# Kernel tuning notes

Measured on AMD Instinct MI355X. Metric: run time of the kernel, lower is better.

Reference implementation:

```python
import jax, jax.numpy as jnp
import numpy as np

N, E, D_IN, D_OUT, R, B = 50000, 800000, 64, 64, 10, 4

def setup_inputs() -> dict:
    key = jax.random.key(0)
    ks = jax.random.split(key, 8)
    feat = jax.random.normal(ks[0], (N, D_IN), jnp.float32)
    src = jax.random.randint(ks[1], (E,), 0, N)
    dst = jax.random.randint(ks[2], (E,), 0, N)
    etype = jax.random.randint(ks[3], (E,), 0, R)
    norm = jax.random.uniform(ks[4], (E,), jnp.float32)
    weight = jax.random.normal(ks[5], (B, D_IN, D_OUT), jnp.float32) * 0.1
    w_comp = jax.random.normal(ks[6], (R, B), jnp.float32) * 0.1
    self_loop_weight = jax.random.normal(ks[7], (D_IN, D_OUT), jnp.float32) * 0.1
    return dict(feat=feat, src=src, dst=dst, etype=etype, norm=norm,
                weight=weight, w_comp=w_comp, self_loop_weight=self_loop_weight)

def reference(feat, src, dst, etype, norm, weight, w_comp, self_loop_weight):
    # Basis decomposition: per-relation weight W_r = sum_b w_comp[r,b] * weight[b]
    W = jnp.einsum('rb,bio->rio', w_comp, weight)            # [R, D_in, D_out]
    # Transform all nodes under every relation (R is small), then gather per edge.
    # This avoids materializing an [E, D_in, D_out] per-edge weight tensor.
    xr = jnp.einsum('ni,rio->rno', feat, W)                  # [R, N, D_out]
    msg = xr[etype, src] * norm[:, None]                     # [E, D_out]
    # Scatter-aggregate messages into destination nodes (DGL sum aggregator).
    agg = jax.ops.segment_sum(msg, dst, num_segments=N)      # [N, D_out]
    # SumAggregator adds curr_emb = dst_feat @ self_loop_weight to the msg sum.
    h = feat @ self_loop_weight + agg                        # [N, D_out]
    return jax.nn.relu(h)
```

## Files before the change

kernel.cpp:

```cpp
#include <hip/hip_runtime.h>
#include <hip/hip_bf16.h>
#include <stdint.h>

#define NN 50000
#define EE 800000
#define DD 64
#define RR 10
#define BB 4
#define NPAD 50176
#define NBKT 391
#define TBLK 4301
#define BBLK 196
#define SORT_CAP 7168
#define FCAP 4096

using u16 = unsigned short;
using u32 = unsigned int;

typedef short v8s __attribute__((ext_vector_type(8)));
typedef float v4f __attribute__((ext_vector_type(4)));

__device__ __forceinline__ u32 f2bf_rn(float x) {
    u32 u = __float_as_uint(x);
    return (u + 0x7FFFu + ((u >> 16) & 1u)) >> 16;
}
__device__ __forceinline__ u32 pack2bf(float a, float b) {
    return f2bf_rn(a) | (f2bf_rn(b) << 16);
}

__global__ __launch_bounds__(256, 2)
void k_big(const float* __restrict__ feat,
           const float* __restrict__ weight,
           const float* __restrict__ w_comp,
           const float* __restrict__ self_w,
           const int* __restrict__ src, const int* __restrict__ dst,
           const int* __restrict__ etype, const float* __restrict__ norm,
           int* __restrict__ bcur, int* __restrict__ flag,
           uint2* __restrict__ rec,
           u16* __restrict__ xr, float* __restrict__ out,
           int tcount, int tb_off, int cap) {
    __shared__ __align__(16) char smem[34816];
    const int t = threadIdx.x;

    if ((int)blockIdx.x >= tcount) {
        int* lh  = (int*)smem;
        int* gb  = lh + 392;
        int* lcc = gb + 392;
        const int ebase = ((int)blockIdx.x - tcount) * 4096;
        for (int b = t; b < 392; b += 256) { lh[b] = 0; lcc[b] = 0; }
        __syncthreads();
        #pragma unroll 4
        for (int j = 0; j < 16; ++j) {
            int e = ebase + t + 256 * j;
            if (e < EE) atomicAdd(&lh[dst[e] >> 7], 1);
        }
        __syncthreads();
        for (int b = t; b < 392; b += 256) {
            int c = lh[b];
            gb[b] = c ? atomicAdd(&bcur[b], c) : 0;
        }
        __syncthreads();
        #pragma unroll 4
        for (int j = 0; j < 16; ++j) {
            int e = ebase + t + 256 * j;
            if (e < EE) {
                int d = dst[e];
                int b = d >> 7;
                int p = atomicAdd(&lcc[b], 1);
                int idx = gb[b] + p;
                u32 w0 = (u32)src[e] | ((u32)etype[e] << 16) | ((u32)(d & 127) << 20);
                if (cap == 0 || idx < (b + 1) * cap)
                    rec[idx] = make_uint2(w0, __float_as_uint(norm[e]));
                else
                    atomicOr(&flag[b], 2);
            }
        }
        return;
    }

    u16*   sWt = (u16*)smem;
    u16*   sFb = (u16*)(smem + 9216);
    float* sD  = (float*)smem;

    const int tb = (int)blockIdx.x + tb_off;
    const int r = tb / 391;
    const int nbase = (tb % 391) * 128;

    if (r < RR) {
        const float c0 = w_comp[r * BB + 0];
        const float c1 = w_comp[r * BB + 1];
        const float c2 = w_comp[r * BB + 2];
        const float c3 = w_comp[r * BB + 3];
        #pragma unroll
        for (int qq = 0; qq < 16; ++qq) {
            int idx = t + 256 * qq;
            int n = idx & 63, k = idx >> 6;
            float v = c0 * weight[k * 64 + n] + c1 * weight[4096 + k * 64 + n] +
                      c2 * weight[8192 + k * 64 + n] + c3 * weight[12288 + k * 64 + n];
            sWt[n * 72 + k] = (u16)f2bf_rn(v);
        }
    } else {
        #pragma unroll
        for (int qq = 0; qq < 16; ++qq) {
            int idx = t + 256 * qq;
            int n = idx & 63, k = idx >> 6;
            sWt[n * 72 + k] = (u16)f2bf_rn(self_w[k * 64 + n]);
        }
    }

    #pragma unroll
    for (int qq = 0; qq < 8; ++qq) {
        int f4 = qq * 256 + t;
        int nl = f4 >> 4;
        int ic = (f4 & 15) << 2;
        int n = nbase + nl;
        float4 v = make_float4(0.f, 0.f, 0.f, 0.f);
        if (n < NN) v = reinterpret_cast<const float4*>(feat)[(size_t)n * 16 + (f4 & 15)];
        *reinterpret_cast<uint2*>(&sFb[nl * 72 + ic]) =
            make_uint2(pack2bf(v.x, v.y), pack2bf(v.z, v.w));
    }
    __syncthreads();

    const int wv = t >> 6;
    const int L = t & 63;
    const int q = L >> 4;
    const int c = L & 15;

    v8s bf[4][2];
    #pragma unroll
    for (int nt = 0; nt < 4; ++nt)
        #pragma unroll
        for (int kh = 0; kh < 2; ++kh)
            bf[nt][kh] = *reinterpret_cast<const v8s*>(&sWt[(nt * 16 + c) * 72 + kh * 32 + q * 8]);

    v8s af[2][2];
    #pragma unroll
    for (int mt = 0; mt < 2; ++mt) {
        int row = wv * 32 + mt * 16 + c;
        #pragma unroll
        for (int kh = 0; kh < 2; ++kh)
            af[mt][kh] = *reinterpret_cast<const v8s*>(&sFb[row * 72 + kh * 32 + q * 8]);
    }
    __syncthreads();

    v4f acc[2][4];
    #pragma unroll
    for (int mt = 0; mt < 2; ++mt)
        #pragma unroll
        for (int nt = 0; nt < 4; ++nt) {
            acc[mt][nt] = (v4f)(0.f);
            #pragma unroll
            for (int kh = 0; kh < 2; ++kh)
                acc[mt][nt] = __builtin_amdgcn_mfma_f32_16x16x32_bf16(
                    af[mt][kh], bf[nt][kh], acc[mt][nt], 0, 0, 0);
        }

    #pragma unroll
    for (int mt = 0; mt < 2; ++mt) {
        int mrow = wv * 32 + mt * 16 + q * 4;
        #pragma unroll
        for (int nt = 0; nt < 4; ++nt)
            #pragma unroll
            for (int rg = 0; rg < 4; ++rg)
                sD[(mrow + rg) * 68 + nt * 16 + c] = acc[mt][nt][rg];
    }
    __syncthreads();

    const int row = t >> 1;
    const int cb = (t & 1) * 32;
    const int g = nbase + row;
    if (g < NN) {
        const float* sp = &sD[row * 68 + cb];
        if (r < RR) {
            u16* dp = xr + ((size_t)r * NN + g) * DD + cb;
            #pragma unroll
            for (int j = 0; j < 4; ++j) {
                float4 f0 = *reinterpret_cast<const float4*>(sp + j * 8);
                float4 f1 = *reinterpret_cast<const float4*>(sp + j * 8 + 4);
                uint4 o;
                o.x = pack2bf(f0.x, f0.y);
                o.y = pack2bf(f0.z, f0.w);
                o.z = pack2bf(f1.x, f1.y);
                o.w = pack2bf(f1.z, f1.w);
                *reinterpret_cast<uint4*>(dp + j * 8) = o;
            }
        } else {
            float* dp = out + (size_t)g * DD + cb;
            #pragma unroll
            for (int j = 0; j < 8; ++j)
                *reinterpret_cast<float4*>(dp + j * 4) =
                    *reinterpret_cast<const float4*>(sp + j * 4);
        }
    }
}

__global__ __launch_bounds__(256)
void k_init(int* __restrict__ bcur, int* __restrict__ flag) {
    int t = blockIdx.x * 256 + threadIdx.x;
    if (t < 392) { bcur[t] = t * FCAP; flag[t] = 0; }
}

__global__ __launch_bounds__(256)
void k_bhist(const int* __restrict__ dst, int* __restrict__ bktcnt) {
    __shared__ int lh[NBKT];
    const int t = threadIdx.x;
    for (int b = t; b < NBKT; b += 256) lh[b] = 0;
    __syncthreads();
    const int ebase = blockIdx.x * 8192;
    #pragma unroll
    for (int j = 0; j < 32; ++j) {
        int e = ebase + t + 256 * j;
        if (e < EE) atomicAdd(&lh[dst[e] >> 7], 1);
    }
    __syncthreads();
    for (int b = t; b < NBKT; b += 256) {
        int v = lh[b];
        if (v) atomicAdd(&bktcnt[b], v);
    }
}

__global__ __launch_bounds__(512)
void k_bscan(const int* __restrict__ bktcnt, int* __restrict__ bktbase,
             int* __restrict__ bcur, int* __restrict__ flag) {
    __shared__ int s[512];
    int t = threadIdx.x;
    int v = (t < NBKT) ? bktcnt[t] : 0;
    s[t] = v;
    __syncthreads();
    #pragma unroll
    for (int off = 1; off < 512; off <<= 1) {
        int x = (t >= off) ? s[t - off] : 0;
        __syncthreads();
        s[t] += x;
        __syncthreads();
    }
    if (t < 392) {
        int b = s[t] - v;
        bktbase[t] = b;
        bcur[t] = b;
        flag[t] = 0;
    }
}

__global__ __launch_bounds__(512)
void k_sortb2(const int* __restrict__ bcurF, const int* __restrict__ bktbase,
              int* __restrict__ flag, uint2* __restrict__ rec,
              int* __restrict__ base, int* __restrict__ cnt, int cap) {
    __shared__ uint2 buf[SORT_CAP];
    __shared__ int h[128];
    __shared__ int sc[128];
    __shared__ int lc[128];
    const int b = blockIdx.x;
    const int t = threadIdx.x;
    const int seg0 = cap ? b * cap : bktbase[b];
    const int cnt_b = bcurF[b] - seg0;
    if (flag[b] & 2) return;
    if (cnt_b > SORT_CAP) {
        if (t == 0) flag[b] = 1;
        return;
    }
    if (t < 128) h[t] = 0;
    __syncthreads();
    for (int k = t; k < cnt_b; k += 512) {
        uint2 rr = rec[seg0 + k];
        buf[k] = rr;
        atomicAdd(&h[(rr.x >> 20) & 127], 1);
    }
    __syncthreads();
    if (t < 128) sc[t] = h[t];
    __syncthreads();
    #pragma unroll
    for (int off = 1; off < 128; off <<= 1) {
        int x = 0;
        if (t < 128 && t >= off) x = sc[t - off];
        __syncthreads();
        if (t < 128) sc[t] += x;
        __syncthreads();
    }
    if (t < 128) {
        int ex = sc[t] - h[t];
        lc[t] = ex;
        base[b * 128 + t] = seg0 + ex;
        cnt[b * 128 + t] = h[t];
    }
    __syncthreads();
    for (int k = t; k < cnt_b; k += 512) {
        uint2 rr = buf[k];
        int p = atomicAdd(&lc[(rr.x >> 20) & 127], 1);
        rec[seg0 + p] = rr;
    }
}

__global__ __launch_bounds__(256)
void k_agg(const int* __restrict__ base, const int* __restrict__ cnt,
           const uint2* __restrict__ rec, const u16* __restrict__ xr,
           const int* __restrict__ flag, const int* __restrict__ bktbase,
           const int* __restrict__ bcurF,
           const int* __restrict__ src, const int* __restrict__ dst,
           const int* __restrict__ etype, const float* __restrict__ norm,
           int cap, float* __restrict__ out) {
    int n = (blockIdx.x * 256 + threadIdx.x) >> 6;
    int L = threadIdx.x & 63;
    if (n >= NN) return;
    const int g = L >> 4;
    const int c = L & 15;
    float a0 = 0.f, a1 = 0.f, a2 = 0.f, a3 = 0.f;
    const int fb = flag[n >> 7];

    if (__builtin_expect(fb == 0, 1)) {
        int st = base[n];
        int cn = cnt[n];
        int k = 0;
        for (; k + 16 <= cn; k += 16) {
            uint2 r0 = rec[st + k + g];
            uint2 r1 = rec[st + k + 4 + g];
            uint2 r2 = rec[st + k + 8 + g];
            uint2 r3 = rec[st + k + 12 + g];
            size_t w0 = ((size_t)((r0.x >> 16) & 0xFu) * NN + (r0.x & 0xFFFFu)) * DD;
            size_t w1 = ((size_t)((r1.x >> 16) & 0xFu) * NN + (r1.x & 0xFFFFu)) * DD;
            size_t w2 = ((size_t)((r2.x >> 16) & 0xFu) * NN + (r2.x & 0xFFFFu)) * DD;
            size_t w3 = ((size_t)((r3.x >> 16) & 0xFu) * NN + (r3.x & 0xFFFFu)) * DD;
            uint2 u0 = *reinterpret_cast<const uint2*>(&xr[w0 + 4 * c]);
            uint2 u1 = *reinterpret_cast<const uint2*>(&xr[w1 + 4 * c]);
            uint2 u2 = *reinterpret_cast<const uint2*>(&xr[w2 + 4 * c]);
            uint2 u3 = *reinterpret_cast<const uint2*>(&xr[w3 + 4 * c]);
            float n0 = __uint_as_float(r0.y), n1 = __uint_as_float(r1.y);
            float n2 = __uint_as_float(r2.y), n3 = __uint_as_float(r3.y);
            a0 = fmaf(__uint_as_float((u0.x & 0xFFFFu) << 16), n0, a0);
            a1 = fmaf(__uint_as_float(u0.x & 0xFFFF0000u), n0, a1);
            a2 = fmaf(__uint_as_float((u0.y & 0xFFFFu) << 16), n0, a2);
            a3 = fmaf(__uint_as_float(u0.y & 0xFFFF0000u), n0, a3);
            a0 = fmaf(__uint_as_float((u1.x & 0xFFFFu) << 16), n1, a0);
            a1 = fmaf(__uint_as_float(u1.x & 0xFFFF0000u), n1, a1);
            a2 = fmaf(__uint_as_float((u1.y & 0xFFFFu) << 16), n1, a2);
            a3 = fmaf(__uint_as_float(u1.y & 0xFFFF0000u), n1, a3);
            a0 = fmaf(__uint_as_float((u2.x & 0xFFFFu) << 16), n2, a0);
            a1 = fmaf(__uint_as_float(u2.x & 0xFFFF0000u), n2, a1);
            a2 = fmaf(__uint_as_float((u2.y & 0xFFFFu) << 16), n2, a2);
            a3 = fmaf(__uint_as_float(u2.y & 0xFFFF0000u), n2, a3);
            a0 = fmaf(__uint_as_float((u3.x & 0xFFFFu) << 16), n3, a0);
            a1 = fmaf(__uint_as_float(u3.x & 0xFFFF0000u), n3, a1);
            a2 = fmaf(__uint_as_float((u3.y & 0xFFFFu) << 16), n3, a2);
            a3 = fmaf(__uint_as_float(u3.y & 0xFFFF0000u), n3, a3);
        }
        for (int kk = k + g; kk < cn; kk += 4) {
            uint2 rr = rec[st + kk];
            size_t rw = ((size_t)((rr.x >> 16) & 0xFu) * NN + (rr.x & 0xFFFFu)) * DD;
            uint2 u = *reinterpret_cast<const uint2*>(&xr[rw + 4 * c]);
            float nm = __uint_as_float(rr.y);
            a0 = fmaf(__uint_as_float((u.x & 0xFFFFu) << 16), nm, a0);
            a1 = fmaf(__uint_as_float(u.x & 0xFFFF0000u), nm, a1);
            a2 = fmaf(__uint_as_float((u.y & 0xFFFFu) << 16), nm, a2);
            a3 = fmaf(__uint_as_float(u.y & 0xFFFF0000u), nm, a3);
        }
    } else if (fb & 2) {
        for (int e = g; e < EE; e += 4) {
            if (dst[e] == n) {
                size_t rw = ((size_t)etype[e] * NN + src[e]) * DD;
                uint2 u = *reinterpret_cast<const uint2*>(&xr[rw + 4 * c]);
                float nm = norm[e];
                a0 = fmaf(__uint_as_float((u.x & 0xFFFFu) << 16), nm, a0);
                a1 = fmaf(__uint_as_float(u.x & 0xFFFF0000u), nm, a1);
                a2 = fmaf(__uint_as_float((u.y & 0xFFFFu) << 16), nm, a2);
                a3 = fmaf(__uint_as_float(u.y & 0xFFFF0000u), nm, a3);
            }
        }
    } else {
        int b = n >> 7;
        int seg0 = cap ? b * cap : bktbase[b];
        int segend = bcurF[b];
        int my = n & 127;
        for (int k = seg0 + g; k < segend; k += 4) {
            uint2 rr = rec[k];
            if (((rr.x >> 20) & 127) == (u32)my) {
                size_t rw = ((size_t)((rr.x >> 16) & 0xFu) * NN + (rr.x & 0xFFFFu)) * DD;
                uint2 u = *reinterpret_cast<const uint2*>(&xr[rw + 4 * c]);
                float nm = __uint_as_float(rr.y);
                a0 = fmaf(__uint_as_float((u.x & 0xFFFFu) << 16), nm, a0);
                a1 = fmaf(__uint_as_float(u.x & 0xFFFF0000u), nm, a1);
                a2 = fmaf(__uint_as_float((u.y & 0xFFFFu) << 16), nm, a2);
                a3 = fmaf(__uint_as_float(u.y & 0xFFFF0000u), nm, a3);
            }
        }
    }
    a0 += __shfl_xor(a0, 16); a1 += __shfl_xor(a1, 16);
    a2 += __shfl_xor(a2, 16); a3 += __shfl_xor(a3, 16);
    a0 += __shfl_xor(a0, 32); a1 += __shfl_xor(a1, 32);
    a2 += __shfl_xor(a2, 32); a3 += __shfl_xor(a3, 32);
    if (g == 0) {
        size_t o = (size_t)n * DD + 4 * c;
        float4 v = *reinterpret_cast<const float4*>(&out[o]);
        v.x = fmaxf(v.x + a0, 0.f);
        v.y = fmaxf(v.y + a1, 0.f);
        v.z = fmaxf(v.z + a2, 0.f);
        v.w = fmaxf(v.w + a3, 0.f);
        *reinterpret_cast<float4*>(&out[o]) = v;
    }
}

__global__ __launch_bounds__(256)
void k_edges(const int* __restrict__ src, const int* __restrict__ dst,
             const int* __restrict__ etype, const float* __restrict__ norm,
             const u16* __restrict__ xr, float* __restrict__ out) {
    int gtid = blockIdx.x * 256 + threadIdx.x;
    int e = gtid >> 4;
    int l = gtid & 15;
    if (e >= EE) return;
    int s = src[e];
    int d = dst[e];
    int rt = etype[e];
    float nm = norm[e];
    size_t row = ((size_t)rt * NN + s) * DD;
    uint2 u = *reinterpret_cast<const uint2*>(&xr[row + l * 4]);
    float f0 = __uint_as_float((u.x & 0xFFFFu) << 16);
    float f1 = __uint_as_float(u.x & 0xFFFF0000u);
    float f2 = __uint_as_float((u.y & 0xFFFFu) << 16);
    float f3 = __uint_as_float(u.y & 0xFFFF0000u);
    float* op = out + (size_t)d * DD + l * 4;
    atomicAdd(op + 0, f0 * nm);
    atomicAdd(op + 1, f1 * nm);
    atomicAdd(op + 2, f2 * nm);
    atomicAdd(op + 3, f3 * nm);
}

__global__ void k_makeW(const float* __restrict__ weight,
                        const float* __restrict__ w_comp,
                        float* __restrict__ W) {
    int f = blockIdx.x * 256 + threadIdx.x;
    if (f >= RR * 4096) return;
    int r = f >> 12;
    int io = f & 4095;
    float v = 0.f;
    #pragma unroll
    for (int b = 0; b < BB; ++b) v += w_comp[r * BB + b] * weight[b * 4096 + io];
    W[f] = v;
}

__global__ __launch_bounds__(256)
void k_edges_direct(const int* __restrict__ src, const int* __restrict__ dst,
                    const int* __restrict__ etype, const float* __restrict__ norm,
                    const float* __restrict__ feat, const float* __restrict__ W,
                    float* __restrict__ out) {
    int gtid = blockIdx.x * 256 + threadIdx.x;
    int e = gtid >> 6;
    int lane = gtid & 63;
    if (e >= EE) return;
    int s = src[e];
    int d = dst[e];
    int rt = etype[e];
    float nm = norm[e];
    const float* fr = feat + (size_t)s * DD;
    const float* Wr = W + (size_t)rt * 4096;
    float acc = 0.f;
    #pragma unroll
    for (int i = 0; i < DD; ++i) acc = fmaf(fr[i], Wr[i * DD + lane], acc);
    atomicAdd(&out[(size_t)d * DD + lane], acc * nm);
}

__global__ __launch_bounds__(256)
void k_relu(float* __restrict__ out) {
    int i = blockIdx.x * 256 + threadIdx.x;
    float4* p = reinterpret_cast<float4*>(out);
    float4 v = p[i];
    v.x = fmaxf(v.x, 0.f);
    v.y = fmaxf(v.y, 0.f);
    v.z = fmaxf(v.z, 0.f);
    v.w = fmaxf(v.w, 0.f);
    p[i] = v;
}

extern "C" void kernel_launch(void* const* d_in, const int* in_sizes, int n_in,
                              void* d_out, int out_size, void* d_ws, size_t ws_size,
                              hipStream_t stream) {
    const float* feat   = (const float*)d_in[0];
    const int*   src    = (const int*)d_in[1];
    const int*   dst    = (const int*)d_in[2];
    const int*   etype  = (const int*)d_in[3];
    const float* norm   = (const float*)d_in[4];
    const float* weight = (const float*)d_in[5];
    const float* w_comp = (const float*)d_in[6];
    const float* self_w = (const float*)d_in[7];
    float* out = (float*)d_out;

    const size_t sz_xr     = (size_t)RR * NN * DD * sizeof(u16);
    const size_t off_bkc   = sz_xr;
    const size_t off_bkb   = off_bkc + 1600;
    const size_t off_bcur  = off_bkb + 1600;
    const size_t off_flag  = off_bcur + 1600;
    const size_t off_base  = off_flag + 1600;
    const size_t off_cnt   = off_base + (size_t)NPAD * 4;
    const size_t off_rec   = off_cnt + (size_t)NPAD * 4;
    const size_t need_hist  = off_rec + (size_t)EE * 8;
    const size_t need_fixed = off_rec + (size_t)NBKT * FCAP * 8;

    dim3 blk(256);
    char* ws = (char*)d_ws;

    if (ws_size >= need_hist) {
        u16*  xr      = (u16*)ws;
        int*  bktcnt  = (int*)(ws + off_bkc);
        int*  bktbase = (int*)(ws + off_bkb);
        int*  bcur    = (int*)(ws + off_bcur);
        int*  flag    = (int*)(ws + off_flag);
        int*  basep   = (int*)(ws + off_base);
        int*  cntp    = (int*)(ws + off_cnt);
        uint2* rec    = (uint2*)(ws + off_rec);
        const int cap = (ws_size >= need_fixed) ? FCAP : 0;

        if (cap) {
            k_init<<<dim3(2), blk, 0, stream>>>(bcur, flag);
        } else {
            hipMemsetAsync(bktcnt, 0, 1600, stream);
            k_bhist<<<dim3(98), blk, 0, stream>>>(dst, bktcnt);
            k_bscan<<<dim3(1), dim3(512), 0, stream>>>(bktcnt, bktbase, bcur, flag);
        }
        k_big<<<dim3(TBLK + BBLK), blk, 0, stream>>>(feat, weight, w_comp, self_w,
                                                     src, dst, etype, norm,
                                                     bcur, flag, rec, xr, out,
                                                     TBLK, 0, cap);
        k_sortb2<<<dim3(NBKT), dim3(512), 0, stream>>>(bcur, bktbase, flag, rec,
                                                       basep, cntp, cap);
        k_agg<<<dim3((NN * 64 + 255) / 256), blk, 0, stream>>>(
            basep, cntp, rec, xr, flag, bktbase, bcur,
            src, dst, etype, norm, cap, out);
    } else if (ws_size >= sz_xr) {
        u16* xr = (u16*)d_ws;
        k_big<<<dim3(TBLK), blk, 0, stream>>>(feat, weight, w_comp, self_w,
                                              src, dst, etype, norm,
                                              (int*)d_ws, (int*)d_ws, (uint2*)d_ws,
                                              xr, out, TBLK, 0, 0);
        k_edges<<<dim3(EE * 16 / 256), blk, 0, stream>>>(src, dst, etype, norm, xr, out);
        k_relu<<<dim3(NN * DD / 4 / 256), blk, 0, stream>>>(out);
    } else {
        k_big<<<dim3(391), blk, 0, stream>>>(feat, weight, w_comp, self_w,
                                             src, dst, etype, norm,
                                             (int*)d_ws, (int*)d_ws, (uint2*)d_ws,
                                             (u16*)d_ws, out, 391, 3910, 0);
        float* W = (float*)d_ws;
        k_makeW<<<dim3(160), blk, 0, stream>>>(weight, w_comp, W);
        k_edges_direct<<<dim3(EE * 64 / 256), blk, 0, stream>>>(src, dst, etype, norm,
                                                                feat, W, out);
        k_relu<<<dim3(NN * DD / 4 / 256), blk, 0, stream>>>(out);
    }
}
```

Measured before the change: 178.3 us.

## Pad per-node edge groups to 16, sort via LDS, schedule binning blocks first

Binning blocks now come first in the fused k_big grid, so edge bucketing begins before the transform blocks are scheduled. k_init is replaced by a memset and the per-bucket cursor becomes a local count. k_sortb2 scatters records into an LDS buffer, padding each destination node's group to a multiple of 16 with zero records, then writes the buffer back contiguously. The padding lets the aggregation loop run over aligned, uniform groups, at the cost of extra zero-norm work and more writes.

```diff
diff --git a/kernel.cpp b/kernel.cpp
--- a/kernel.cpp
+++ b/kernel.cpp
@@ -11,7 +11,7 @@
 #define NBKT 391
 #define TBLK 4301
 #define BBLK 196
-#define SORT_CAP 7168
+#define PADCAP 8192
 #define FCAP 4096
 
 using u16 = unsigned short;
@@ -38,15 +38,15 @@
            int* __restrict__ bcur, int* __restrict__ flag,
            uint2* __restrict__ rec,
            u16* __restrict__ xr, float* __restrict__ out,
-           int tcount, int tb_off, int cap) {
+           int nbin, int tb_off, int cap) {
     __shared__ __align__(16) char smem[34816];
     const int t = threadIdx.x;
 
-    if ((int)blockIdx.x >= tcount) {
+    if ((int)blockIdx.x < nbin) {
         int* lh  = (int*)smem;
         int* gb  = lh + 392;
         int* lcc = gb + 392;
-        const int ebase = ((int)blockIdx.x - tcount) * 4096;
+        const int ebase = (int)blockIdx.x * 4096;
         for (int b = t; b < 392; b += 256) { lh[b] = 0; lcc[b] = 0; }
         __syncthreads();
         #pragma unroll 4
@@ -67,12 +67,16 @@
                 int d = dst[e];
                 int b = d >> 7;
                 int p = atomicAdd(&lcc[b], 1);
-                int idx = gb[b] + p;
                 u32 w0 = (u32)src[e] | ((u32)etype[e] << 16) | ((u32)(d & 127) << 20);
-                if (cap == 0 || idx < (b + 1) * cap)
-                    rec[idx] = make_uint2(w0, __float_as_uint(norm[e]));
-                else
-                    atomicOr(&flag[b], 2);
+                if (cap) {
+                    int il = gb[b] + p;
+                    if (il < cap)
+                        rec[(size_t)b * cap + il] = make_uint2(w0, __float_as_uint(norm[e]));
+                    else
+                        atomicOr(&flag[b], 2);
+                } else {
+                    rec[gb[b] + p] = make_uint2(w0, __float_as_uint(norm[e]));
+                }
             }
         }
         return;
@@ -82,7 +86,7 @@
     u16*   sFb = (u16*)(smem + 9216);
     float* sD  = (float*)smem;
 
-    const int tb = (int)blockIdx.x + tb_off;
+    const int tb = (int)blockIdx.x - nbin + tb_off;
     const int r = tb / 391;
     const int nbase = (tb % 391) * 128;
 
@@ -195,12 +199,6 @@
 }
 
 __global__ __launch_bounds__(256)
-void k_init(int* __restrict__ bcur, int* __restrict__ flag) {
-    int t = blockIdx.x * 256 + threadIdx.x;
-    if (t < 392) { bcur[t] = t * FCAP; flag[t] = 0; }
-}
-
-__global__ __launch_bounds__(256)
 void k_bhist(const int* __restrict__ dst, int* __restrict__ bktcnt) {
     __shared__ int lh[NBKT];
     const int t = threadIdx.x;
@@ -246,28 +244,30 @@
 void k_sortb2(const int* __restrict__ bcurF, const int* __restrict__ bktbase,
               int* __restrict__ flag, uint2* __restrict__ rec,
               int* __restrict__ base, int* __restrict__ cnt, int cap) {
-    __shared__ uint2 buf[SORT_CAP];
+    __shared__ uint2 buf[PADCAP];
     __shared__ int h[128];
+    __shared__ int pc[128];
     __shared__ int sc[128];
     __shared__ int lc[128];
+    __shared__ int totp;
     const int b = blockIdx.x;
     const int t = threadIdx.x;
     const int seg0 = cap ? b * cap : bktbase[b];
-    const int cnt_b = bcurF[b] - seg0;
+    const int cnt_b = cap ? bcurF[b] : (bcurF[b] - seg0);
     if (flag[b] & 2) return;
-    if (cnt_b > SORT_CAP) {
+    if (cnt_b > 6144) {
         if (t == 0) flag[b] = 1;
         return;
     }
     if (t < 128) h[t] = 0;
     __syncthreads();
-    for (int k = t; k < cnt_b; k += 512) {
-        uint2 rr = rec[seg0 + k];
-        buf[k] = rr;
-        atomicAdd(&h[(rr.x >> 20) & 127], 1);
-    }
-    __syncthreads();
-    if (t < 128) sc[t] = h[t];
+    for (int k = t; k < cnt_b; k += 512)
+        atomicAdd(&h[(rec[seg0 + k].x >> 20) & 127], 1);
+    __syncthreads();
+    if (t < 128) {
+        pc[t] = cap ? ((h[t] + 15) & ~15) : h[t];
+        sc[t] = pc[t];
+    }
     __syncthreads();
     #pragma unroll
     for (int off = 1; off < 128; off <<= 1) {
@@ -277,18 +277,29 @@
         if (t < 128) sc[t] += x;
         __syncthreads();
     }
+    if (t == 127) totp = sc[127];
+    __syncthreads();
+    const int total = totp;
+    if (total > PADCAP || (cap && total > cap)) {
+        if (t == 0) flag[b] = 1;
+        return;
+    }
     if (t < 128) {
-        int ex = sc[t] - h[t];
+        int ex = sc[t] - pc[t];
         lc[t] = ex;
         base[b * 128 + t] = seg0 + ex;
-        cnt[b * 128 + t] = h[t];
-    }
+        cnt[b * 128 + t] = pc[t];
+    }
+    for (int k = t; k < total; k += 512) buf[k] = make_uint2(0u, 0u);
     __syncthreads();
     for (int k = t; k < cnt_b; k += 512) {
-        uint2 rr = buf[k];
+        uint2 rr = rec[seg0 + k];
         int p = atomicAdd(&lc[(rr.x >> 20) & 127], 1);
-        rec[seg0 + p] = rr;
-    }
+        buf[p] = rr;
+    }
+    __syncthreads();
+    for (int k = t; k < total; k += 512)
+        rec[seg0 + k] = buf[k];
 }
 
 __global__ __launch_bounds__(256)
@@ -368,7 +379,7 @@
     } else {
         int b = n >> 7;
         int seg0 = cap ? b * cap : bktbase[b];
-        int segend = bcurF[b];
+        int segend = cap ? (b * cap + bcurF[b]) : bcurF[b];
         int my = n & 127;
         for (int k = seg0 + g; k < segend; k += 4) {
             uint2 rr = rec[k];
@@ -507,17 +518,15 @@
         uint2* rec    = (uint2*)(ws + off_rec);
         const int cap = (ws_size >= need_fixed) ? FCAP : 0;
 
-        if (cap) {
-            k_init<<<dim3(2), blk, 0, stream>>>(bcur, flag);
-        } else {
-            hipMemsetAsync(bktcnt, 0, 1600, stream);
+        hipMemsetAsync(bktcnt, 0, 6400, stream);
+        if (!cap) {
             k_bhist<<<dim3(98), blk, 0, stream>>>(dst, bktcnt);
             k_bscan<<<dim3(1), dim3(512), 0, stream>>>(bktcnt, bktbase, bcur, flag);
         }
         k_big<<<dim3(TBLK + BBLK), blk, 0, stream>>>(feat, weight, w_comp, self_w,
                                                      src, dst, etype, norm,
                                                      bcur, flag, rec, xr, out,
-                                                     TBLK, 0, cap);
+                                                     BBLK, 0, cap);
         k_sortb2<<<dim3(NBKT), dim3(512), 0, stream>>>(bcur, bktbase, flag, rec,
                                                        basep, cntp, cap);
         k_agg<<<dim3((NN * 64 + 255) / 256), blk, 0, stream>>>(
@@ -528,14 +537,14 @@
         k_big<<<dim3(TBLK), blk, 0, stream>>>(feat, weight, w_comp, self_w,
                                               src, dst, etype, norm,
                                               (int*)d_ws, (int*)d_ws, (uint2*)d_ws,
-                                              xr, out, TBLK, 0, 0);
+                                              xr, out, 0, 0, 0);
         k_edges<<<dim3(EE * 16 / 256), blk, 0, stream>>>(src, dst, etype, norm, xr, out);
         k_relu<<<dim3(NN * DD / 4 / 256), blk, 0, stream>>>(out);
     } else {
         k_big<<<dim3(391), blk, 0, stream>>>(feat, weight, w_comp, self_w,
                                              src, dst, etype, norm,
                                              (int*)d_ws, (int*)d_ws, (uint2*)d_ws,
-                                             (u16*)d_ws, out, 391, 3910, 0);
+                                             (u16*)d_ws, out, 0, 3910, 0);
         float* W = (float*)d_ws;
         k_makeW<<<dim3(160), blk, 0, stream>>>(weight, w_comp, W);
         k_edges_direct<<<dim3(EE * 64 / 256), blk, 0, stream>>>(src, dst, etype, norm,
```

Result: faster. 168.2 us, median of 2 (-5.7%).
